# Optimization experiments

Measured on AMD Instinct MI355X. Metric: run time of the kernel, lower is better.

Reference implementation:

```python
import jax, jax.numpy as jnp
import numpy as np
import math

POOL_H = 8
POOL_W = 16
LATENT_H = 48
LATENT_W = 80
VISUAL_LEN = 7680   # 2 frames of 48*80 latent tokens
SPARSITY = 0.9
NUM_HEADS = 16
HEAD_DIM = 64


def _reorg_restore():
    # part/block/sub-block token reorganization so pooled sub-blocks are contiguous
    part = LATENT_W * POOL_H          # 640
    blk = LATENT_W                    # 80
    sub = POOL_W                      # 16
    bpp = part // blk                 # blocks per part = 8
    spb = blk // sub                  # sub-blocks per block = 5
    # orig index = b*blk + c*sub + i ; new order iterates (c, b, i)
    pat = np.arange(part).reshape(bpp, spb, sub).transpose(1, 0, 2).reshape(-1)
    nparts = VISUAL_LEN // part
    reorg = (np.arange(nparts)[:, None] * part + pat[None, :]).reshape(-1)
    restore = np.argsort(reorg)       # inverse permutation
    return jnp.asarray(reorg), jnp.asarray(restore)

REORG_IDX, RESTORE_IDX = _reorg_restore()


def _draft_attn_map(q, k):
    # q, k: [L, H, D] -> pooled attention map [H, S, S]
    L, H, D = q.shape
    nf = L // (LATENT_H * LATENT_W)
    def pool(x):
        # 2D avg-pool each frame (dims divide exactly -> reshape+mean)
        x = x.reshape(nf, LATENT_H // POOL_H, POOL_H, LATENT_W // POOL_W, POOL_W, H, D)
        return x.mean(axis=(2, 4)).reshape(-1, H, D)   # [S, H, D]
    qs, ks = pool(q), pool(k)
    scores = jnp.einsum('lhd,mhd->hlm', qs, ks) / math.sqrt(D)
    return jax.nn.softmax(scores, axis=-1)


def _percentile_mask(attn, r):
    # keep top-r fraction of entries per head: threshold = max of k smallest
    H, S, _ = attn.shape
    n = S * S
    kk = int((1.0 - r) * n)           # number of entries dropped (0 < kk < n here)
    thr = jnp.sort(attn.reshape(H, n), axis=-1)[:, kk - 1]
    return attn >= thr[:, None, None]


def _head_attn(qh, kh, vh, mblk):
    # qh/kh/vh: [L, D]; mblk: [nb, nb] bool block mask, block size L//nb (=128)
    L, D = qh.shape
    nb = mblk.shape[0]
    mB = L // nb
    s = (qh @ kh.T) * (1.0 / math.sqrt(D))              # [L, L]
    s = jnp.where(mblk[:, None, :, None], s.reshape(nb, mB, nb, mB), -jnp.inf)
    s = s.reshape(L, L)
    m = jnp.max(s, axis=-1, keepdims=True)
    m = jnp.where(jnp.isfinite(m), m, 0.0)              # fully-masked rows -> 0 output
    p = jnp.exp(s - m)                                  # exp(-inf) = 0
    p = p / jnp.maximum(p.sum(-1, keepdims=True), 1e-30)
    return p @ vh


def _forward(q, k, v, batch_size, max_seqlen_q):
    attn = _draft_attn_map(q, k)                        # [H, S, S]
    mask = _percentile_mask(attn, 1.0 - SPARSITY)       # [H, S, S] bool
    qr, kr, vr = q[REORG_IDX], k[REORG_IDX], v[REORG_IDX]
    qh = jnp.swapaxes(qr, 0, 1)                         # [H, L, D]
    kh = jnp.swapaxes(kr, 0, 1)
    vh = jnp.swapaxes(vr, 0, 1)
    f = jax.checkpoint(lambda t: _head_attn(*t))
    out = jax.lax.map(f, (qh, kh, vh, mask))            # sequential over heads: [H, L, D]
    x = jnp.swapaxes(out, 0, 1)[RESTORE_IDX]            # [L, H, D]
    return x.reshape(batch_size, max_seqlen_q, q.shape[1], q.shape[2])


def setup_inputs() -> dict:
    key = jax.random.key(0)
    kq, kk, kv = jax.random.split(key, 3)
    L = VISUAL_LEN
    q = jax.random.normal(kq, (L, NUM_HEADS, HEAD_DIM), dtype=jnp.float32)
    k = jax.random.normal(kk, (L, NUM_HEADS, HEAD_DIM), dtype=jnp.float32)
    v = jax.random.normal(kv, (L, NUM_HEADS, HEAD_DIM), dtype=jnp.float32)
    return {
        'q': q, 'k': k, 'v': v,
        'cu_seqlens_q': jnp.array([0, L], dtype=jnp.int32),
        'cu_seqlens_kv': jnp.array([0, L], dtype=jnp.int32),
        'max_seqlen_q': L,
        'max_seqlen_kv': L,
        'batch_size': 1,
    }


def reference(q, k, v, cu_seqlens_q, cu_seqlens_kv, max_seqlen_q, max_seqlen_kv, batch_size):
    return _forward(q, k, v, batch_size, max_seqlen_q)
```

## Files before the change

kernel.cpp:

```cpp
#include <hip/hip_runtime.h>

#define L_TOK   7680
#define NHEAD   16
#define HDIM    64
#define NBLK    60
#define KEEP    361
#define QS_OFF   0u
#define KS_OFF   491520u
#define CNT_OFF  983040u
#define COL_OFF  986880u
#define KHM_OFF  1217280u
#define VTM_OFF  16945920u

typedef short bf16x8 __attribute__((ext_vector_type(8)));
typedef short bf16x4 __attribute__((ext_vector_type(4)));
typedef float f32x4  __attribute__((ext_vector_type(4)));

__device__ __forceinline__ unsigned int cvtpk(float lo, float hi) {
  unsigned int r;
  asm("v_cvt_pk_bf16_f32 %0, %1, %2" : "=v"(r) : "v"(lo), "v"(hi));
  return r;
}

__device__ __forceinline__ f32x4 mfma16(bf16x4 a, bf16x4 b, f32x4 c) {
#if __has_builtin(__builtin_amdgcn_mfma_f32_16x16x16bf16_1k)
  return __builtin_amdgcn_mfma_f32_16x16x16bf16_1k(a, b, c, 0, 0, 0);
#else
  asm("v_mfma_f32_16x16x16_bf16 %0, %1, %2, %0" : "+v"(c) : "v"(a), "v"(b));
  return c;
#endif
}

__device__ __forceinline__ void gll16(const unsigned short* gsrc, unsigned short* ldst) {
  __builtin_amdgcn_global_load_lds(
      (const __attribute__((address_space(1))) unsigned int*)gsrc,
      (__attribute__((address_space(3))) unsigned int*)ldst, 16, 0, 0);
}

__global__ __launch_bounds__(256) void prep_kernel(
    const float* __restrict__ qin, const float* __restrict__ kin,
    const float* __restrict__ vin, double* __restrict__ qs, double* __restrict__ ks,
    unsigned short* __restrict__ khm, unsigned short* __restrict__ vtm) {
  __shared__ float stg[128 * 68];
  __shared__ double psum[4][64];
  const int h = blockIdx.x, blk = blockIdx.y, t = threadIdx.x;
  const int p = blk / 5, c = blk % 5;
  const int q4 = t >> 6, dq = t & 63;

  unsigned short* kdst = khm + (size_t)(h * 60 + blk) * 8192;
  #pragma unroll
  for (int it = 0; it < 4; ++it) {
    int sidx = it * 256 + t;  int row = sidx >> 3, s = sidx & 7;
    int tok = p * 640 + (row >> 4) * 80 + c * 16 + (row & 15);
    const float* src = kin + (size_t)tok * 1024 + h * 64 + s * 8;
    float4 a = ((const float4*)src)[0], b = ((const float4*)src)[1];
    uint4 un; un.x = cvtpk(a.x, a.y); un.y = cvtpk(a.z, a.w);
    un.z = cvtpk(b.x, b.y); un.w = cvtpk(b.z, b.w);
    *(uint4*)(kdst + row * 64 + ((s ^ (row & 7)) * 8)) = un;
    *(float4*)&stg[row * 68 + s * 8] = a;
    *(float4*)&stg[row * 68 + s * 8 + 4] = b;
  }
  __syncthreads();
  { double acc = 0.0;
    for (int r = 0; r < 32; ++r) acc += (double)stg[(q4 * 32 + r) * 68 + dq];
    psum[q4][dq] = acc; }
  __syncthreads();
  if (t < 64)
    ks[(size_t)(h * 60 + blk) * 64 + t] =
        (psum[0][t] + psum[1][t] + psum[2][t] + psum[3][t]) * (1.0 / 128.0);
  __syncthreads();

  #pragma unroll
  for (int it = 0; it < 4; ++it) {
    int sidx = it * 256 + t;  int row = sidx >> 3, s = sidx & 7;
    int tok = p * 640 + (row >> 4) * 80 + c * 16 + (row & 15);
    const float* src = qin + (size_t)tok * 1024 + h * 64 + s * 8;
    float4 a = ((const float4*)src)[0], b = ((const float4*)src)[1];
    *(float4*)&stg[row * 68 + s * 8] = a;
    *(float4*)&stg[row * 68 + s * 8 + 4] = b;
  }
  __syncthreads();
  { double acc = 0.0;
    for (int r = 0; r < 32; ++r) acc += (double)stg[(q4 * 32 + r) * 68 + dq];
    psum[q4][dq] = acc; }
  __syncthreads();
  if (t < 64)
    qs[(size_t)(h * 60 + blk) * 64 + t] =
        (psum[0][t] + psum[1][t] + psum[2][t] + psum[3][t]) * (1.0 / 128.0);
  __syncthreads();

  #pragma unroll
  for (int it = 0; it < 8; ++it) {
    int idx = it * 256 + t;  int row = idx >> 4, f4 = idx & 15;
    int tok = p * 640 + (row >> 4) * 80 + c * 16 + (row & 15);
    float4 a = ((const float4*)(vin + (size_t)tok * 1024 + h * 64))[f4];
    *(float4*)&stg[row * 68 + f4 * 4] = a;
  }
  __syncthreads();
  unsigned short* vdst = vtm + (size_t)(h * 60 + blk) * 8192;
  #pragma unroll
  for (int it = 0; it < 4; ++it) {
    int u = it * 256 + t;  int d = u >> 4, sl = u & 15;
    int kbase = (sl >> 2) * 32 + (sl & 3) * 4;
    uint4 un;
    un.x = cvtpk(stg[(kbase + 0) * 68 + d],  stg[(kbase + 1) * 68 + d]);
    un.y = cvtpk(stg[(kbase + 2) * 68 + d],  stg[(kbase + 3) * 68 + d]);
    un.z = cvtpk(stg[(kbase + 16) * 68 + d], stg[(kbase + 17) * 68 + d]);
    un.w = cvtpk(stg[(kbase + 18) * 68 + d], stg[(kbase + 19) * 68 + d]);
    *(uint4*)(vdst + d * 128 + ((sl ^ (d & 7)) * 8)) = un;
  }
}

__global__ void scores_kernel(const double* __restrict__ qs, const double* __restrict__ ks,
                              float* __restrict__ probsF) {
  const int i = blockIdx.x, h = blockIdx.y, j = threadIdx.x;
  const double* qr = qs + (size_t)(h * 60 + i) * 64;
  double sc = -1.0e300;
  if (j < 60) {
    const double* kr = ks + (size_t)(h * 60 + j) * 64;
    double a0 = 0, a1 = 0, a2 = 0, a3 = 0;
    #pragma unroll
    for (int d = 0; d < 64; d += 4) {
      a0 += qr[d]     * kr[d];
      a1 += qr[d + 1] * kr[d + 1];
      a2 += qr[d + 2] * kr[d + 2];
      a3 += qr[d + 3] * kr[d + 3];
    }
    sc = ((a0 + a1) + (a2 + a3)) * 0.125;
  }
  double m = sc;
  #pragma unroll
  for (int o = 32; o; o >>= 1) m = fmax(m, __shfl_xor(m, o, 64));
  double e = (j < 60) ? exp(sc - m) : 0.0;
  double ssum = e;
  #pragma unroll
  for (int o = 32; o; o >>= 1) ssum += __shfl_xor(ssum, o, 64);
  if (j < 60) probsF[(size_t)(h * 60 + i) * 60 + j] = (float)(e / ssum);
}

__global__ __launch_bounds__(256) void select_kernel(const float* __restrict__ probsF,
                                                     int* __restrict__ counts,
                                                     int* __restrict__ cols) {
  const int h = blockIdx.x, t = threadIdx.x;
  __shared__ float pb[3600];
  __shared__ int hist[2048];
  __shared__ int warr[4];
  __shared__ int sh_digit, sh_above;

  unsigned int myv[15];
  #pragma unroll
  for (int m2 = 0; m2 < 15; ++m2) {
    int i = t + m2 * 256;
    float v = 0.0f;
    if (i < 3600) { v = probsF[(size_t)h * 3600 + i]; pb[i] = v; }
    myv[m2] = __float_as_uint(v);
  }
  __syncthreads();

  unsigned int prefix = 0;
  int rank = KEEP;
  const int lane = t & 63, w = t >> 6;
  #pragma unroll
  for (int pass = 0; pass < 3; ++pass) {
    const int shift = (pass == 0) ? 21 : (pass == 1) ? 10 : 0;
    const int width = (pass == 2) ? 10 : 11;
    const int dmask = (1 << width) - 1;
    for (int i = t; i < 2048; i += 256) hist[i] = 0;
    __syncthreads();
    const int hb = shift + width;
    #pragma unroll
    for (int m2 = 0; m2 < 15; ++m2) {
      unsigned int u = myv[m2];
      if (u && (pass == 0 || (u >> hb) == (prefix >> hb)))
        atomicAdd(&hist[(int)((u >> shift) & dmask)], 1);
    }
    __syncthreads();
    const int base = t * 8;
    int bcnt[8], s = 0;
    #pragma unroll
    for (int b = 0; b < 8; ++b) { bcnt[b] = hist[base + b]; s += bcnt[b]; }
    int incl = s;
    #pragma unroll
    for (int o = 1; o < 64; o <<= 1) {
      int y = __shfl_down(incl, o, 64);
      if (lane + o < 64) incl += y;
    }
    if (lane == 0) warr[w] = incl;
    __syncthreads();
    int above_w = 0;
    for (int w2 = w + 1; w2 < 4; ++w2) above_w += warr[w2];
    int run = (incl - s) + above_w;
    #pragma unroll
    for (int b = 7; b >= 0; --b) {
      int c = bcnt[b];
      if (c > 0 && run < rank && run + c >= rank) { sh_digit = base + b; sh_above = run; }
      run += c;
    }
    __syncthreads();
    prefix |= ((unsigned int)sh_digit) << shift;
    rank -= sh_above;
    __syncthreads();
  }

  const float thr = __uint_as_float(prefix);
  if (t < 60) {
    int cnt = 0;
    int tmp[60];
    for (int j = 0; j < 60; ++j)
      if (pb[t * 60 + j] >= thr) tmp[cnt++] = j;
    for (int j = 0; j < cnt; ++j) cols[(size_t)(h * 60 + t) * 60 + j] = tmp[j];
    counts[h * 60 + t] = cnt;
  }
}

__global__ __launch_bounds__(256, 2) void attn_kernel(
    const float* __restrict__ qin, const unsigned short* __restrict__ khm,
    const unsigned short* __restrict__ vtm, const int* __restrict__ counts,
    const int* __restrict__ cols, float* __restrict__ out) {
  const int h = blockIdx.x, qb = blockIdx.y;
  const int t = threadIdx.x, w = t >> 6, lane = t & 63;
  const int g = lane >> 4, n = lane & 15, sw = n & 7;
  __shared__ __align__(16) float LDSf[128 * 68];
  unsigned short* Kt = (unsigned short*)LDSf;
  unsigned short* Vt = (unsigned short*)LDSf + 8192;

  const int cnt = counts[h * 60 + qb];
  const int pq = qb / 5, cq = qb % 5;
  if (cnt == 0) {
    for (int i = t; i < 2048; i += 256) {
      int row = i >> 4, f4 = i & 15;
      int tok = pq * 640 + (row >> 4) * 80 + cq * 16 + (row & 15);
      float4 z = {0.f, 0.f, 0.f, 0.f};
      *(float4*)(out + (size_t)tok * 1024 + h * 64 + f4 * 4) = z;
    }
    return;
  }

  const int* mycols = cols + (size_t)(h * 60 + qb) * 60;
  int colv = mycols[lane < cnt ? lane : 0];

  bf16x8 aq[2][2];
  #pragma unroll
  for (int qt = 0; qt < 2; ++qt) {
    int lq = w * 32 + qt * 16 + n;
    int tok = pq * 640 + (lq >> 4) * 80 + cq * 16 + (lq & 15);
    const float* qrow = qin + (size_t)tok * 1024 + h * 64;
    #pragma unroll
    for (int hh = 0; hh < 2; ++hh) {
      const float4* s4 = (const float4*)(qrow + hh * 32 + g * 8);
      float4 a = s4[0], b2 = s4[1];
      union { bf16x8 v; unsigned int uw[4]; } un;
      un.uw[0] = cvtpk(a.x, a.y);  un.uw[1] = cvtpk(a.z, a.w);
      un.uw[2] = cvtpk(b2.x, b2.y); un.uw[3] = cvtpk(b2.z, b2.w);
      aq[qt][hh] = un.v;
    }
  }

  const f32x4 zero4 = {0.f, 0.f, 0.f, 0.f};
  f32x4 acco[2][4];
  float mst[2] = {-1.0e38f, -1.0e38f}, lst[2] = {0.f, 0.f};
  #pragma unroll
  for (int qt = 0; qt < 2; ++qt)
    #pragma unroll
    for (int dt = 0; dt < 4; ++dt) acco[qt][dt] = zero4;

  const unsigned short* khm_h = khm + (size_t)(h * 60) * 8192;
  const unsigned short* vtm_h = vtm + (size_t)(h * 60) * 8192;
  const float C2 = 0.18033688011112042f;

  for (int ki = 0; ki < cnt; ++ki) {
    const int kb = __shfl(colv, ki, 64);
    __syncthreads();
    {
      const unsigned short* ksrc = khm_h + (size_t)kb * 8192;
      const unsigned short* vsrc = vtm_h + (size_t)kb * 8192;
      #pragma unroll
      for (int j = 0; j < 4; ++j) {
        gll16(ksrc + (size_t)((w * 4 + j) * 512) + lane * 8, Kt + (w * 4 + j) * 512);
        gll16(vsrc + (size_t)((w * 4 + j) * 512) + lane * 8, Vt + (w * 4 + j) * 512);
      }
    }
    asm volatile("s_waitcnt vmcnt(0)" ::: "memory");
    __syncthreads();

    f32x4 accs[2][8];
    #pragma unroll
    for (int qt = 0; qt < 2; ++qt)
      #pragma unroll
      for (int kt = 0; kt < 8; ++kt) accs[qt][kt] = zero4;
    __builtin_amdgcn_s_setprio(1);
    #pragma unroll
    for (int kt = 0; kt < 8; ++kt) {
      int rowbase = (kt * 16 + n) * 64;
      bf16x8 k0 = *(const bf16x8*)&Kt[rowbase + ((g ^ sw) * 8)];
      bf16x8 k1 = *(const bf16x8*)&Kt[rowbase + (((4 + g) ^ sw) * 8)];
      accs[0][kt] = __builtin_amdgcn_mfma_f32_16x16x32_bf16(k0, aq[0][0], accs[0][kt], 0, 0, 0);
      accs[0][kt] = __builtin_amdgcn_mfma_f32_16x16x32_bf16(k1, aq[0][1], accs[0][kt], 0, 0, 0);
      accs[1][kt] = __builtin_amdgcn_mfma_f32_16x16x32_bf16(k0, aq[1][0], accs[1][kt], 0, 0, 0);
      accs[1][kt] = __builtin_amdgcn_mfma_f32_16x16x32_bf16(k1, aq[1][1], accs[1][kt], 0, 0, 0);
    }
    __builtin_amdgcn_s_setprio(0);

    bf16x4 pbv[2][8];
    #pragma unroll
    for (int qt = 0; qt < 2; ++qt) {
      float mloc = -1.0e38f;
      #pragma unroll
      for (int kt = 0; kt < 8; ++kt) {
        float m01 = fmaxf(fmaxf(accs[qt][kt][0], accs[qt][kt][1]),
                          fmaxf(accs[qt][kt][2], accs[qt][kt][3]));
        mloc = fmaxf(mloc, m01);
      }
      mloc = fmaxf(mloc, __shfl_xor(mloc, 16, 64));
      mloc = fmaxf(mloc, __shfl_xor(mloc, 32, 64));
      float mn = fmaxf(mst[qt], mloc * C2);
      float fsq = __builtin_amdgcn_exp2f(mst[qt] - mn);
      mst[qt] = mn;
      float rs0 = 0.f, rs1 = 0.f, rs2 = 0.f, rs3 = 0.f;
      #pragma unroll
      for (int kt = 0; kt < 8; ++kt) {
        float p0 = __builtin_amdgcn_exp2f(fmaf(accs[qt][kt][0], C2, -mn));
        float p1 = __builtin_amdgcn_exp2f(fmaf(accs[qt][kt][1], C2, -mn));
        float p2 = __builtin_amdgcn_exp2f(fmaf(accs[qt][kt][2], C2, -mn));
        float p3 = __builtin_amdgcn_exp2f(fmaf(accs[qt][kt][3], C2, -mn));
        rs0 += p0; rs1 += p1; rs2 += p2; rs3 += p3;
        union { unsigned int u[2]; bf16x4 v; } pb;
        pb.u[0] = cvtpk(p0, p1);
        pb.u[1] = cvtpk(p2, p3);
        pbv[qt][kt] = pb.v;
      }
      float rsum = (rs0 + rs1) + (rs2 + rs3);
      rsum += __shfl_xor(rsum, 16, 64);
      rsum += __shfl_xor(rsum, 32, 64);
      lst[qt] = lst[qt] * fsq + rsum;
      #pragma unroll
      for (int dt = 0; dt < 4; ++dt)
        #pragma unroll
        for (int r = 0; r < 4; ++r) acco[qt][dt][r] *= fsq;
    }

    __builtin_amdgcn_s_setprio(1);
    #pragma unroll
    for (int kp = 0; kp < 4; ++kp) {
      #pragma unroll
      for (int dt = 0; dt < 4; ++dt) {
        int d = dt * 16 + n;
        bf16x8 vv = *(const bf16x8*)&Vt[d * 128 + (((kp * 4 + g) ^ sw) * 8)];
        bf16x4 vlo = __builtin_shufflevector(vv, vv, 0, 1, 2, 3);
        bf16x4 vhi = __builtin_shufflevector(vv, vv, 4, 5, 6, 7);
        acco[0][dt] = mfma16(vlo, pbv[0][2 * kp],     acco[0][dt]);
        acco[0][dt] = mfma16(vhi, pbv[0][2 * kp + 1], acco[0][dt]);
        acco[1][dt] = mfma16(vlo, pbv[1][2 * kp],     acco[1][dt]);
        acco[1][dt] = mfma16(vhi, pbv[1][2 * kp + 1], acco[1][dt]);
      }
    }
    __builtin_amdgcn_s_setprio(0);
  }

  __syncthreads();
  #pragma unroll
  for (int qt = 0; qt < 2; ++qt) {
    float inv = 1.0f / lst[qt];
    int q = w * 32 + qt * 16 + n;
    #pragma unroll
    for (int dt = 0; dt < 4; ++dt)
      #pragma unroll
      for (int r = 0; r < 4; ++r)
        LDSf[q * 68 + dt * 16 + 4 * g + r] = acco[qt][dt][r] * inv;
  }
  __syncthreads();
  for (int i = t; i < 2048; i += 256) {
    int q = i >> 4, f4 = i & 15;
    int tok = pq * 640 + (q >> 4) * 80 + cq * 16 + (q & 15);
    float4 val = *(float4*)&LDSf[q * 68 + f4 * 4];
    *(float4*)(out + (size_t)tok * 1024 + h * 64 + f4 * 4) = val;
  }
}

extern "C" void kernel_launch(void* const* d_in, const int* in_sizes, int n_in,
                              void* d_out, int out_size, void* d_ws, size_t ws_size,
                              hipStream_t stream) {
  const float* qin = (const float*)d_in[0];
  const float* kin = (const float*)d_in[1];
  const float* vin = (const float*)d_in[2];
  char* ws = (char*)d_ws;
  double* qs = (double*)(ws + QS_OFF);
  double* ks = (double*)(ws + KS_OFF);
  int* counts = (int*)(ws + CNT_OFF);
  int* cols = (int*)(ws + COL_OFF);
  float* probsF = (float*)(ws + COL_OFF);
  unsigned short* khm = (unsigned short*)(ws + KHM_OFF);
  unsigned short* vtm = (unsigned short*)(ws + VTM_OFF);
  float* outp = (float*)d_out;

  prep_kernel<<<dim3(16, 60), 256, 0, stream>>>(qin, kin, vin, qs, ks, khm, vtm);
  scores_kernel<<<dim3(60, 16), 64, 0, stream>>>(qs, ks, probsF);
  select_kernel<<<16, 256, 0, stream>>>(probsF, counts, cols);
  attn_kernel<<<dim3(16, 60), 256, 0, stream>>>(qin, khm, vtm, counts, cols, outp);
}
```

Before: 105.6 us.

## Double-buffer K/V block loads and schedule query blocks by descending work

The attention kernel now uses two LDS buffers for K and V and issues the global-to-LDS loads for the next selected key block while the current one is being computed, waiting only on the older loads. The select kernel also computes, per head, an ordering of query blocks by descending kept-block count, and attn_kernel reads that order so the heaviest blocks are dispatched first. This aims to hide memory latency and reduce tail imbalance. The cost is double the LDS (64KB per block), which may lower occupancy below the two blocks per CU declared in the launch bounds.

```diff
diff --git a/kernel.cpp b/kernel.cpp
--- a/kernel.cpp
+++ b/kernel.cpp
@@ -11,6 +11,7 @@
 #define COL_OFF  986880u
 #define KHM_OFF  1217280u
 #define VTM_OFF  16945920u
+#define ORD_OFF  32674560u
 
 typedef short bf16x8 __attribute__((ext_vector_type(8)));
 typedef short bf16x4 __attribute__((ext_vector_type(4)));
@@ -140,12 +141,14 @@
 
 __global__ __launch_bounds__(256) void select_kernel(const float* __restrict__ probsF,
                                                      int* __restrict__ counts,
-                                                     int* __restrict__ cols) {
+                                                     int* __restrict__ cols,
+                                                     int* __restrict__ order) {
   const int h = blockIdx.x, t = threadIdx.x;
   __shared__ float pb[3600];
   __shared__ int hist[2048];
   __shared__ int warr[4];
   __shared__ int sh_digit, sh_above;
+  __shared__ int scnt[60];
 
   unsigned int myv[15];
   #pragma unroll
@@ -210,19 +213,31 @@
       if (pb[t * 60 + j] >= thr) tmp[cnt++] = j;
     for (int j = 0; j < cnt; ++j) cols[(size_t)(h * 60 + t) * 60 + j] = tmp[j];
     counts[h * 60 + t] = cnt;
+    scnt[t] = cnt;
+  }
+  __syncthreads();
+  if (t < 60) {
+    int c = scnt[t], rk = 0;
+    for (int j = 0; j < 60; ++j) {
+      int cj = scnt[j];
+      rk += (cj > c) || (cj == c && j < t);
+    }
+    order[h * 60 + rk] = t;
   }
 }
 
 __global__ __launch_bounds__(256, 2) void attn_kernel(
     const float* __restrict__ qin, const unsigned short* __restrict__ khm,
     const unsigned short* __restrict__ vtm, const int* __restrict__ counts,
-    const int* __restrict__ cols, float* __restrict__ out) {
-  const int h = blockIdx.x, qb = blockIdx.y;
+    const int* __restrict__ cols, const int* __restrict__ order,
+    float* __restrict__ out) {
+  const int h = blockIdx.x;
+  const int qb = order[h * 60 + blockIdx.y];
   const int t = threadIdx.x, w = t >> 6, lane = t & 63;
   const int g = lane >> 4, n = lane & 15, sw = n & 7;
-  __shared__ __align__(16) float LDSf[128 * 68];
-  unsigned short* Kt = (unsigned short*)LDSf;
-  unsigned short* Vt = (unsigned short*)LDSf + 8192;
+  __shared__ __align__(16) unsigned short LDSb[32768];
+  #define KT(b) (LDSb + (b) * 8192)
+  #define VT(b) (LDSb + 16384 + (b) * 8192)
 
   const int cnt = counts[h * 60 + qb];
   const int pq = qb / 5, cq = qb % 5;
@@ -268,19 +283,33 @@
   const unsigned short* vtm_h = vtm + (size_t)(h * 60) * 8192;
   const float C2 = 0.18033688011112042f;
 
+  {
+    int kb0 = __shfl(colv, 0, 64);
+    asm volatile("s_waitcnt vmcnt(0)" ::: "memory");
+    const unsigned short* ksrc = khm_h + (size_t)kb0 * 8192;
+    const unsigned short* vsrc = vtm_h + (size_t)kb0 * 8192;
+    #pragma unroll
+    for (int j = 0; j < 4; ++j) {
+      gll16(ksrc + (size_t)((w * 4 + j) * 512) + lane * 8, KT(0) + (w * 4 + j) * 512);
+      gll16(vsrc + (size_t)((w * 4 + j) * 512) + lane * 8, VT(0) + (w * 4 + j) * 512);
+    }
+  }
+
   for (int ki = 0; ki < cnt; ++ki) {
-    const int kb = __shfl(colv, ki, 64);
-    __syncthreads();
-    {
-      const unsigned short* ksrc = khm_h + (size_t)kb * 8192;
-      const unsigned short* vsrc = vtm_h + (size_t)kb * 8192;
+    const int b = ki & 1;
+    if (ki + 1 < cnt) {
+      int kbn = __shfl(colv, ki + 1, 64);
+      const unsigned short* ksrc = khm_h + (size_t)kbn * 8192;
+      const unsigned short* vsrc = vtm_h + (size_t)kbn * 8192;
       #pragma unroll
       for (int j = 0; j < 4; ++j) {
-        gll16(ksrc + (size_t)((w * 4 + j) * 512) + lane * 8, Kt + (w * 4 + j) * 512);
-        gll16(vsrc + (size_t)((w * 4 + j) * 512) + lane * 8, Vt + (w * 4 + j) * 512);
+        gll16(ksrc + (size_t)((w * 4 + j) * 512) + lane * 8, KT(b ^ 1) + (w * 4 + j) * 512);
+        gll16(vsrc + (size_t)((w * 4 + j) * 512) + lane * 8, VT(b ^ 1) + (w * 4 + j) * 512);
       }
-    }
-    asm volatile("s_waitcnt vmcnt(0)" ::: "memory");
+      asm volatile("s_waitcnt vmcnt(8)" ::: "memory");
+    } else {
+      asm volatile("s_waitcnt vmcnt(0)" ::: "memory");
+    }
     __syncthreads();
 
     f32x4 accs[2][8];
@@ -292,8 +321,8 @@
     #pragma unroll
     for (int kt = 0; kt < 8; ++kt) {
       int rowbase = (kt * 16 + n) * 64;
-      bf16x8 k0 = *(const bf16x8*)&Kt[rowbase + ((g ^ sw) * 8)];
-      bf16x8 k1 = *(const bf16x8*)&Kt[rowbase + (((4 + g) ^ sw) * 8)];
+      bf16x8 k0 = *(const bf16x8*)&KT(b)[rowbase + ((g ^ sw) * 8)];
+      bf16x8 k1 = *(const bf16x8*)&KT(b)[rowbase + (((4 + g) ^ sw) * 8)];
       accs[0][kt] = __builtin_amdgcn_mfma_f32_16x16x32_bf16(k0, aq[0][0], accs[0][kt], 0, 0, 0);
       accs[0][kt] = __builtin_amdgcn_mfma_f32_16x16x32_bf16(k1, aq[0][1], accs[0][kt], 0, 0, 0);
       accs[1][kt] = __builtin_amdgcn_mfma_f32_16x16x32_bf16(k0, aq[1][0], accs[1][kt], 0, 0, 0);
@@ -345,7 +374,7 @@
       #pragma unroll
       for (int dt = 0; dt < 4; ++dt) {
         int d = dt * 16 + n;
-        bf16x8 vv = *(const bf16x8*)&Vt[d * 128 + (((kp * 4 + g) ^ sw) * 8)];
+        bf16x8 vv = *(const bf16x8*)&VT(b)[d * 128 + (((kp * 4 + g) ^ sw) * 8)];
         bf16x4 vlo = __builtin_shufflevector(vv, vv, 0, 1, 2, 3);
         bf16x4 vhi = __builtin_shufflevector(vv, vv, 4, 5, 6, 7);
         acco[0][dt] = mfma16(vlo, pbv[0][2 * kp],     acco[0][dt]);
@@ -355,9 +384,10 @@
       }
     }
     __builtin_amdgcn_s_setprio(0);
-  }
-
-  __syncthreads();
+    __syncthreads();
+  }
+
+  float* Ot = (float*)LDSb;
   #pragma unroll
   for (int qt = 0; qt < 2; ++qt) {
     float inv = 1.0f / lst[qt];
@@ -366,15 +396,17 @@
     for (int dt = 0; dt < 4; ++dt)
       #pragma unroll
       for (int r = 0; r < 4; ++r)
-        LDSf[q * 68 + dt * 16 + 4 * g + r] = acco[qt][dt][r] * inv;
+        Ot[q * 68 + dt * 16 + 4 * g + r] = acco[qt][dt][r] * inv;
   }
   __syncthreads();
   for (int i = t; i < 2048; i += 256) {
     int q = i >> 4, f4 = i & 15;
     int tok = pq * 640 + (q >> 4) * 80 + cq * 16 + (q & 15);
-    float4 val = *(float4*)&LDSf[q * 68 + f4 * 4];
+    float4 val = *(float4*)&Ot[q * 68 + f4 * 4];
     *(float4*)(out + (size_t)tok * 1024 + h * 64 + f4 * 4) = val;
   }
+  #undef KT
+  #undef VT
 }
 
 extern "C" void kernel_launch(void* const* d_in, const int* in_sizes, int n_in,
@@ -391,10 +423,11 @@
   float* probsF = (float*)(ws + COL_OFF);
   unsigned short* khm = (unsigned short*)(ws + KHM_OFF);
   unsigned short* vtm = (unsigned short*)(ws + VTM_OFF);
+  int* order = (int*)(ws + ORD_OFF);
   float* outp = (float*)d_out;
 
   prep_kernel<<<dim3(16, 60), 256, 0, stream>>>(qin, kin, vin, qs, ks, khm, vtm);
   scores_kernel<<<dim3(60, 16), 64, 0, stream>>>(qs, ks, probsF);
-  select_kernel<<<16, 256, 0, stream>>>(probsF, counts, cols);
-  attn_kernel<<<dim3(16, 60), 256, 0, stream>>>(qin, khm, vtm, counts, cols, outp);
-}
+  select_kernel<<<16, 256, 0, stream>>>(probsF, counts, cols, order);
+  attn_kernel<<<dim3(16, 60), 256, 0, stream>>>(qin, khm, vtm, counts, cols, order, outp);
+}
```

New measurement: 96.28 us. 1.1x faster.
